# Performance work log

Hardware: AMD Instinct MI355X
Metric: run time of the kernel (lower is better)

Reference implementation:

```python
import jax, jax.numpy as jnp
import numpy as np
import math

B, T, D = 4, 4096, 1024
H, M = 16, 64
Dh = D // H


def _rope_tables(head_dim, max_seq_len, base=10000):
    inv_freq = 1.0 / (base ** (np.arange(0, head_dim, 2, dtype=np.float32) / head_dim))
    t = np.arange(max_seq_len, dtype=np.float32)
    freqs = np.einsum('i,j->ij', t, inv_freq)  # [T, Dh/2]
    cos = np.cos(freqs)
    sin = np.sin(freqs)
    # interleave (c, c) pairwise -> [T, Dh]
    cos = np.stack((cos, cos), axis=-1).reshape(max_seq_len, head_dim)
    sin = np.stack((sin, sin), axis=-1).reshape(max_seq_len, head_dim)
    return jnp.asarray(cos), jnp.asarray(sin)


def setup_inputs() -> dict:
    key = jax.random.key(0)
    ks = jax.random.split(key, 6)
    s = 1.0 / math.sqrt(D)
    x = jax.random.normal(ks[0], (B, T, D), dtype=jnp.float32)
    Wq = jnp.clip(jax.random.normal(ks[1], (D, D)) * s, -2 * s, 2 * s).astype(jnp.float32)
    Wk = jnp.clip(jax.random.normal(ks[2], (D, D)) * s, -2 * s, 2 * s).astype(jnp.float32)
    Wv = jnp.clip(jax.random.normal(ks[3], (D, D)) * s, -2 * s, 2 * s).astype(jnp.float32)
    Wo = jnp.clip(jax.random.normal(ks[4], (D, D)) * s, -2 * s, 2 * s).astype(jnp.float32)
    latent_code = (jax.random.normal(ks[5], (H, M, Dh)) * 0.02).astype(jnp.float32)
    rope_cos, rope_sin = _rope_tables(Dh, T)
    mask = jnp.ones((B, 1, T, 1), dtype=jnp.int32)
    return {'x': x, 'Wq': Wq, 'Wk': Wk, 'Wv': Wv, 'Wo': Wo,
            'latent_code': latent_code, 'rope_cos': rope_cos,
            'rope_sin': rope_sin, 'mask': mask}


def _rotate(x):
    # (x1, x2) pairs -> (-x2, x1), interleaved
    x2 = x.reshape(*x.shape[:-1], -1, 2)
    return jnp.stack((-x2[..., 1], x2[..., 0]), axis=-1).reshape(x.shape)


def reference(x, Wq, Wk, Wv, Wo, latent_code, rope_cos, rope_sin, mask):
    Bc, Tc, Dc = x.shape
    scale = 1.0 / math.sqrt(Dh)
    # projections -> [B, H, T, Dh]
    q = (x @ Wq.T).reshape(Bc, Tc, H, Dh).transpose(0, 2, 1, 3)
    k = (x @ Wk.T).reshape(Bc, Tc, H, Dh).transpose(0, 2, 1, 3)
    v = (x @ Wv.T).reshape(Bc, Tc, H, Dh).transpose(0, 2, 1, 3)
    cos = rope_cos[:Tc][None, None]  # [1,1,T,Dh]
    sin = rope_sin[:Tc][None, None]
    q = q * cos + _rotate(q) * sin
    k = k * cos + _rotate(k) * sin
    # Stage 1: token -> latent assignment, softmax over tokens (axis=2)
    assign_logits = jnp.einsum('bhtd,hmd->bhtm', k, latent_code) * scale
    assign_logits = jnp.where(mask == 0, -jnp.inf, assign_logits)
    assign = jax.nn.softmax(assign_logits, axis=2)
    k_lat = jnp.einsum('bhtm,bhtd->bhmd', assign, k)
    v_lat = jnp.einsum('bhtm,bhtd->bhmd', assign, v)
    # Stage 2: query attends to latents, softmax over latents (axis=-1)
    att2 = jnp.einsum('bhtd,bhmd->bhtm', q, k_lat) * scale
    p2 = jax.nn.softmax(att2, axis=-1)
    out = jnp.einsum('bhtm,bhmd->bhtd', p2, v_lat)
    out = out.transpose(0, 2, 1, 3).reshape(Bc, Tc, Dc)
    return out @ Wo.T
```

## Files before the change

kernel.cpp:

```cpp
#include <hip/hip_runtime.h>
#include <hip/hip_bf16.h>
#include <stdint.h>


#define DEV static __device__ __forceinline__

using short8 = __attribute__((ext_vector_type(8))) short;
using f32x4  = __attribute__((ext_vector_type(4))) float;

#define ZERO4 (f32x4){0.f, 0.f, 0.f, 0.f}

DEV float bf2f(unsigned short u) {
  union { unsigned int i; float f; } c; c.i = ((unsigned int)u) << 16; return c.f;
}
DEV unsigned short f2bf(float f) {
  __hip_bfloat16 h = __float2bfloat16(f);
  unsigned short u; __builtin_memcpy(&u, &h, 2); return u;
}
DEV f32x4 mfma16(short8 a, short8 b, f32x4 c) {
  return __builtin_amdgcn_mfma_f32_16x16x32_bf16(a, b, c, 0, 0, 0);
}
#define GLOAD_LDS16(G, L) __builtin_amdgcn_global_load_lds( \
    (const __attribute__((address_space(1))) void*)(G),     \
    (__attribute__((address_space(3))) void*)(L), 16, 0, 0)

__global__ void cvt_all(const float* __restrict__ x,
                        const float* __restrict__ Wq, const float* __restrict__ Wk,
                        const float* __restrict__ Wv, const float* __restrict__ Wo,
                        __hip_bfloat16* __restrict__ xb,
                        __hip_bfloat16* __restrict__ Wb) {
  const int bid = blockIdx.x;
  const float* src;
  __hip_bfloat16* dst;
  int base;
  if (bid < 16384) {
    src = x; dst = xb; base = bid;
  } else {
    const int k = (bid - 16384) >> 10;
    src = (k == 0) ? Wq : (k == 1) ? Wk : (k == 2) ? Wv : Wo;
    dst = Wb + (size_t)k * 1048576;
    base = (bid - 16384) & 1023;
  }
  const int i = (base * 256 + threadIdx.x) * 4;
  const float4 v = *(const float4*)(src + i);
  ushort4 o;
  o.x = f2bf(v.x); o.y = f2bf(v.y); o.z = f2bf(v.z); o.w = f2bf(v.w);
  *(ushort4*)(dst + i) = o;
}

#define GEMM_CORE(A_, B_, K_)                                                     \
  __shared__ __hip_bfloat16 As[2][256 * 64];                                      \
  __shared__ __hip_bfloat16 Bs[2][256 * 64];                                      \
  const int tid = threadIdx.x;                                                    \
  const int w = tid >> 6, l = tid & 63;                                           \
  const int lr = l & 15, lg = l >> 4;                                             \
  const int rowA0 = blockIdx.x * 256;                                             \
  const int colB0 = blockIdx.y * 256;                                             \
  const int srow = w * 8 + (l >> 3);                                              \
  const int skk  = (((l & 7) ^ (l >> 3)) * 8);                                    \
  const __hip_bfloat16* Ab = A_ + (size_t)(rowA0 + srow) * K_ + skk;              \
  const __hip_bfloat16* Bb = B_ + (size_t)(colB0 + srow) * K_ + skk;              \
  f32x4 acc[8][4];                                                                \
  _Pragma("unroll")                                                               \
  for (int i = 0; i < 8; ++i)                                                     \
    _Pragma("unroll")                                                             \
    for (int j = 0; j < 4; ++j) acc[i][j] = ZERO4;                                \
  const int wr = (w >> 2) * 128;                                                  \
  const int wc = (w & 3) * 64;                                                    \
  const int NT = K_ >> 6;                                                         \
  {                                                                               \
    const int k0s = 0;                                                            \
    _Pragma("unroll")                                                             \
    for (int i = 0; i < 4; ++i) {                                                 \
      GLOAD_LDS16(Ab + (size_t)(i * 64) * K_ + k0s, &As[0][i * 4096 + w * 512]);  \
      GLOAD_LDS16(Bb + (size_t)(i * 64) * K_ + k0s, &Bs[0][i * 4096 + w * 512]);  \
    }                                                                             \
  }                                                                               \
  for (int kt = 0; kt < NT; ++kt) {                                               \
    const int cur = kt & 1;                                                       \
    if (kt + 1 < NT) {                                                            \
      const int k0s = (kt + 1) * 64;                                              \
      _Pragma("unroll")                                                           \
      for (int i = 0; i < 4; ++i) {                                               \
        GLOAD_LDS16(Ab + (size_t)(i * 64) * K_ + k0s, &As[cur ^ 1][i * 4096 + w * 512]); \
        GLOAD_LDS16(Bb + (size_t)(i * 64) * K_ + k0s, &Bs[cur ^ 1][i * 4096 + w * 512]); \
      }                                                                           \
      asm volatile("s_waitcnt vmcnt(8)" ::: "memory");                            \
    } else {                                                                      \
      asm volatile("s_waitcnt vmcnt(0)" ::: "memory");                            \
    }                                                                             \
    __builtin_amdgcn_s_barrier();                                                 \
    __builtin_amdgcn_s_setprio(1);                                                \
    _Pragma("unroll")                                                             \
    for (int s = 0; s < 2; ++s) {                                                 \
      short8 fa[8], fb[4];                                                        \
      _Pragma("unroll")                                                           \
      for (int i = 0; i < 8; ++i)                                                 \
        fa[i] = *(const short8*)&As[cur][(wr + i * 16 + lr) * 64 +                \
                                         (((s * 4 + lg) ^ (lr & 7)) * 8)];        \
      _Pragma("unroll")                                                           \
      for (int j = 0; j < 4; ++j)                                                 \
        fb[j] = *(const short8*)&Bs[cur][(wc + j * 16 + lr) * 64 +                \
                                         (((s * 4 + lg) ^ (lr & 7)) * 8)];        \
      _Pragma("unroll")                                                           \
      for (int i = 0; i < 8; ++i)                                                 \
        _Pragma("unroll")                                                         \
        for (int j = 0; j < 4; ++j)                                               \
          acc[i][j] = mfma16(fa[i], fb[j], acc[i][j]);                            \
    }                                                                             \
    __builtin_amdgcn_s_setprio(0);                                                \
    __builtin_amdgcn_s_barrier();                                                 \
  }

__global__ __launch_bounds__(512, 2)
void gemm_qkv(const __hip_bfloat16* __restrict__ A,
              const __hip_bfloat16* __restrict__ Bt,
              __hip_bfloat16* __restrict__ qb,
              __hip_bfloat16* __restrict__ kb,
              __hip_bfloat16* __restrict__ kT,
              __hip_bfloat16* __restrict__ vT,
              const float* __restrict__ cosT, const float* __restrict__ sinT) {
  GEMM_CORE(A, Bt, 1024)
  const int r0 = rowA0 + wr + lg * 4;
  const int c0 = colB0 + wc + lr;
  const int panel = blockIdx.y >> 2;
  if (panel < 2) {
#pragma unroll
    for (int i = 0; i < 8; ++i)
#pragma unroll
      for (int j = 0; j < 4; ++j)
#pragma unroll
        for (int r = 0; r < 4; ++r) {
          const int m = r0 + i * 16 + r;
          const int n = c0 + j * 16;
          const int t = m & 4095, d = n & 63;
          const float c = cosT[t * 64 + d];
          const float s = sinT[t * 64 + d];
          const float v = acc[i][j][r];
          const float other = __shfl_xor(v, 1, 64);
          acc[i][j][r] = v * c + ((n & 1) ? other : -other) * s;
        }
  }
  if (panel < 2) {
    __hip_bfloat16* Cn = (panel == 0) ? qb : kb;
#pragma unroll
    for (int i = 0; i < 8; ++i)
#pragma unroll
      for (int j = 0; j < 4; ++j)
#pragma unroll
        for (int r = 0; r < 4; ++r) {
          const int nn = (c0 + j * 16) & 1023;
          Cn[(size_t)(r0 + i * 16 + r) * 1024 + nn] = __float2bfloat16(acc[i][j][r]);
        }
  }
  if (panel >= 1) {
    __hip_bfloat16* Ct = (panel == 1) ? kT : vT;
#pragma unroll
    for (int i = 0; i < 8; ++i)
#pragma unroll
      for (int j = 0; j < 4; ++j) {
        const int m0 = r0 + i * 16;
        const int nn = (c0 + j * 16) & 1023;
        const size_t row = (size_t)(((m0 >> 12) * 16 + (nn >> 6)) * 64 + (nn & 63));
        ushort4 pk;
        pk.x = f2bf(acc[i][j][0]); pk.y = f2bf(acc[i][j][1]);
        pk.z = f2bf(acc[i][j][2]); pk.w = f2bf(acc[i][j][3]);
        *(ushort4*)&Ct[row * 4096 + (m0 & 4095)] = pk;
      }
  }
}

__global__ __launch_bounds__(512, 2)
void gemm_out(const __hip_bfloat16* __restrict__ A,
              const __hip_bfloat16* __restrict__ Bt,
              float* __restrict__ Cout) {
  GEMM_CORE(A, Bt, 1024)
  const int r0 = rowA0 + wr + lg * 4;
  const int c0 = colB0 + wc + lr;
#pragma unroll
  for (int i = 0; i < 8; ++i)
#pragma unroll
    for (int j = 0; j < 4; ++j)
#pragma unroll
      for (int r = 0; r < 4; ++r)
        Cout[(size_t)(r0 + i * 16 + r) * 1024 + (c0 + j * 16)] = acc[i][j][r];
}

__global__ __launch_bounds__(256)
void stage1_expS(const __hip_bfloat16* __restrict__ kmat,
                 const float* __restrict__ latent,
                 const int* __restrict__ mask,
                 __hip_bfloat16* __restrict__ P,
                 float* __restrict__ psum) {
  const int bh = blockIdx.x, chunk = blockIdx.y;
  const int b = bh >> 4, h = bh & 15;
  const int tid = threadIdx.x, w = tid >> 6, l = tid & 63;
  const int lr = l & 15, lg = l >> 4;
  short8 la[4][2];
#pragma unroll
  for (int n = 0; n < 4; ++n)
#pragma unroll
    for (int s = 0; s < 2; ++s) {
      const float* lp = &latent[((size_t)h * 64 + n * 16 + lr) * 64 + s * 32 + lg * 8];
      short8 f;
#pragma unroll
      for (int j = 0; j < 8; ++j) f[j] = (short)f2bf(lp[j]);
      la[n][s] = f;
    }
  float sm[16];
#pragma unroll
  for (int i = 0; i < 16; ++i) sm[i] = 0.f;
  for (int tile = 0; tile < 8; ++tile) {
    const int t = chunk * 512 + tile * 64 + w * 16 + lr;
    const __hip_bfloat16* kp = &kmat[((size_t)(b * 4096 + t) * 16 + h) * 64 + lg * 8];
    const short8 kb0 = *(const short8*)kp;
    const short8 kb1 = *(const short8*)(kp + 32);
    const bool live = (mask[b * 4096 + t] != 0);
    f32x4 acc[4];
#pragma unroll
    for (int n = 0; n < 4; ++n) {
      acc[n] = ZERO4;
      acc[n] = mfma16(la[n][0], kb0, acc[n]);
      acc[n] = mfma16(la[n][1], kb1, acc[n]);
    }
#pragma unroll
    for (int n = 0; n < 4; ++n)
#pragma unroll
      for (int r = 0; r < 4; ++r) {
        const float e = live ? __expf(acc[n][r] * 0.125f) : 0.f;
        const int m = n * 16 + lg * 4 + r;
        ((unsigned short*)P)[((size_t)bh * 64 + m) * 4096 + t] = f2bf(e);
        sm[n * 4 + r] += e;
      }
  }
#pragma unroll
  for (int o = 1; o < 16; o <<= 1)
#pragma unroll
    for (int i = 0; i < 16; ++i) sm[i] += __shfl_xor(sm[i], o, 64);
  if (lr == 0) {
    const size_t pb = ((size_t)(bh * 8 + chunk) * 4 + w) * 64;
#pragma unroll
    for (int n = 0; n < 4; ++n)
#pragma unroll
      for (int r = 0; r < 4; ++r)
        psum[pb + n * 16 + lg * 4 + r] = sm[n * 4 + r];
  }
}

__global__ void denom_inv(const float* __restrict__ psum, float* __restrict__ cinv) {
  const int i = blockIdx.x * 256 + threadIdx.x;
  if (i >= 4096) return;
  const int bh = i >> 6, m = i & 63;
  float sm = 0.f;
#pragma unroll
  for (int c = 0; c < 32; ++c)
    sm += psum[((size_t)bh * 32 + c) * 64 + m];
  cinv[i] = 1.f / sm;
}

__global__ __launch_bounds__(256)
void latgemm7(const __hip_bfloat16* __restrict__ P,
              const __hip_bfloat16* __restrict__ kT,
              const __hip_bfloat16* __restrict__ vT,
              float* __restrict__ partials) {
  const int bh = blockIdx.x;
  const int tid = threadIdx.x, w = tid >> 6, l = tid & 63;
  const int slice = blockIdx.y * 4 + w;
  const int lr = l & 15;
  const int lk = (l >> 4) * 8;
  const size_t base = (size_t)bh * 64 * 4096;
  f32x4 ak[4][4], av[4][4];
#pragma unroll
  for (int i = 0; i < 4; ++i)
#pragma unroll
    for (int j = 0; j < 4; ++j) { ak[i][j] = ZERO4; av[i][j] = ZERO4; }
  for (int ks = 0; ks < 8; ++ks) {
    const int t = slice * 256 + ks * 32 + lk;
    short8 fp[4], fk[4], fv[4];
#pragma unroll
    for (int i = 0; i < 4; ++i) {
      const size_t ro = base + (size_t)(i * 16 + lr) * 4096 + t;
      fp[i] = *(const short8*)&P[ro];
      fk[i] = *(const short8*)&kT[ro];
      fv[i] = *(const short8*)&vT[ro];
    }
#pragma unroll
    for (int i = 0; i < 4; ++i)
#pragma unroll
      for (int j = 0; j < 4; ++j) {
        ak[i][j] = mfma16(fp[i], fk[j], ak[i][j]);
        av[i][j] = mfma16(fv[i], fp[j], av[i][j]);
      }
  }
  float* pk = partials + ((size_t)(slice * 64 + bh)) * 8192;
#pragma unroll
  for (int i = 0; i < 4; ++i)
#pragma unroll
    for (int j = 0; j < 4; ++j)
#pragma unroll
      for (int r = 0; r < 4; ++r) {
        const int row = i * 16 + 4 * (l >> 4) + r;
        const int col = j * 16 + lr;
        pk[(size_t)row * 64 + col]        = ak[i][j][r];
        pk[4096 + (size_t)row * 64 + col] = av[i][j][r];
      }
}

__global__ void latreduce2(const float* __restrict__ partials,
                           const float* __restrict__ cinv,
                           __hip_bfloat16* __restrict__ k_lat,
                           __hip_bfloat16* __restrict__ v_latT) {
  const int i = blockIdx.x * 256 + threadIdx.x;
  const int bh = i >> 13, off = i & 8191;
  float sm = 0.f;
#pragma unroll
  for (int c = 0; c < 16; ++c)
    sm += partials[((size_t)(c * 64 + bh)) * 8192 + off];
  const int m = (off < 4096) ? (off >> 6) : (off & 63);
  sm *= cinv[bh * 64 + m];
  if (off < 4096) k_lat[(size_t)bh * 4096 + off] = __float2bfloat16(sm);
  else            v_latT[(size_t)bh * 4096 + (off - 4096)] = __float2bfloat16(sm);
}

__global__ __launch_bounds__(256)
void stage2_attn(const __hip_bfloat16* __restrict__ q,
                 const __hip_bfloat16* __restrict__ k_lat,
                 const __hip_bfloat16* __restrict__ v_latT,
                 __hip_bfloat16* __restrict__ attn) {
  __shared__ unsigned short Pl[4][16][64];
  const int bid = blockIdx.x;
  const int bh = bid >> 6, tt = (bid & 63) * 64;
  const int b = bh >> 4, h = bh & 15;
  const int tid = threadIdx.x, w = tid >> 6, l = tid & 63;
  const size_t qoff = ((size_t)(b * 4096 + tt + w * 16 + (l & 15)) * 16 + h) * 64;
  const short8 a0 = *(const short8*)&q[qoff + (l >> 4) * 8];
  const short8 a1 = *(const short8*)&q[qoff + 32 + (l >> 4) * 8];
  f32x4 att[4];
#pragma unroll
  for (int n = 0; n < 4; ++n) att[n] = ZERO4;
#pragma unroll
  for (int n = 0; n < 4; ++n) {
    const __hip_bfloat16* kl = &k_lat[((size_t)bh * 64 + n * 16 + (l & 15)) * 64];
    const short8 b0 = *(const short8*)&kl[(l >> 4) * 8];
    const short8 b1 = *(const short8*)&kl[32 + (l >> 4) * 8];
    att[n] = mfma16(a0, b0, att[n]);
    att[n] = mfma16(a1, b1, att[n]);
  }
  float p[4][4];
#pragma unroll
  for (int r = 0; r < 4; ++r) {
    const float v0 = att[0][r] * 0.125f, v1 = att[1][r] * 0.125f;
    const float v2 = att[2][r] * 0.125f, v3 = att[3][r] * 0.125f;
    float mxv = fmaxf(fmaxf(v0, v1), fmaxf(v2, v3));
#pragma unroll
    for (int o = 1; o < 16; o <<= 1) mxv = fmaxf(mxv, __shfl_xor(mxv, o, 64));
    const float e0 = __expf(v0 - mxv), e1 = __expf(v1 - mxv);
    const float e2 = __expf(v2 - mxv), e3 = __expf(v3 - mxv);
    float sum = e0 + e1 + e2 + e3;
#pragma unroll
    for (int o = 1; o < 16; o <<= 1) sum += __shfl_xor(sum, o, 64);
    const float inv = 1.f / sum;
    p[0][r] = e0 * inv; p[1][r] = e1 * inv; p[2][r] = e2 * inv; p[3][r] = e3 * inv;
  }
#pragma unroll
  for (int n = 0; n < 4; ++n)
#pragma unroll
    for (int r = 0; r < 4; ++r) {
      const int row = 4 * (l >> 4) + r;
      const int col = n * 16 + (l & 15);
      Pl[w][row][col ^ ((row & 7) << 3)] = f2bf(p[n][r]);
    }
  __syncthreads();
  const int arow = l & 15;
  const short8 pa0 = *(const short8*)&Pl[w][arow][(((l >> 4) + 0) ^ (arow & 7)) * 8];
  const short8 pa1 = *(const short8*)&Pl[w][arow][(((l >> 4) + 4) ^ (arow & 7)) * 8];
  f32x4 ov[4];
#pragma unroll
  for (int n = 0; n < 4; ++n) ov[n] = ZERO4;
#pragma unroll
  for (int n = 0; n < 4; ++n) {
    const __hip_bfloat16* vt = &v_latT[((size_t)bh * 64 + n * 16 + (l & 15)) * 64];
    const short8 b0 = *(const short8*)&vt[(l >> 4) * 8];
    const short8 b1 = *(const short8*)&vt[32 + (l >> 4) * 8];
    ov[n] = mfma16(pa0, b0, ov[n]);
    ov[n] = mfma16(pa1, b1, ov[n]);
  }
#pragma unroll
  for (int n = 0; n < 4; ++n) {
    const int d = n * 16 + (l & 15);
#pragma unroll
    for (int r = 0; r < 4; ++r) {
      const int trow = tt + w * 16 + 4 * (l >> 4) + r;
      attn[((size_t)(b * 4096 + trow) * 16 + h) * 64 + d] = __float2bfloat16(ov[n][r]);
    }
  }
}

extern "C" void kernel_launch(void* const* d_in, const int* in_sizes, int n_in,
                              void* d_out, int out_size, void* d_ws, size_t ws_size,
                              hipStream_t stream) {
  const float* x      = (const float*)d_in[0];
  const float* Wq     = (const float*)d_in[1];
  const float* Wk     = (const float*)d_in[2];
  const float* Wv     = (const float*)d_in[3];
  const float* Wo     = (const float*)d_in[4];
  const float* latent = (const float*)d_in[5];
  const float* cosT   = (const float*)d_in[6];
  const float* sinT   = (const float*)d_in[7];
  const int*   mask   = (const int*)d_in[8];

  char* ws = (char*)d_ws;
  __hip_bfloat16* xb = (__hip_bfloat16*)ws;
  __hip_bfloat16* Wb = (__hip_bfloat16*)(ws + 33554432);
  __hip_bfloat16* qb = (__hip_bfloat16*)(ws + 41943040);
  __hip_bfloat16* kb = (__hip_bfloat16*)(ws + 75497472);
  __hip_bfloat16* kT = (__hip_bfloat16*)(ws + 109051904);
  __hip_bfloat16* vT = (__hip_bfloat16*)(ws + 142606336);
  char* tail = ws + 176160768;
  float* psum = (float*)tail;
  float* cinv = psum + 131072;
  __hip_bfloat16* k_lat  = (__hip_bfloat16*)(cinv + 4096);
  __hip_bfloat16* v_latT = k_lat + 262144;
  float* partials = (float*)kb;
  __hip_bfloat16* P    = xb;
  __hip_bfloat16* attn = qb;

  cvt_all<<<20480, 256, 0, stream>>>(x, Wq, Wk, Wv, Wo, xb, Wb);

  dim3 gq(64, 12);
  gemm_qkv<<<gq, 512, 0, stream>>>(xb, Wb, qb, kb, kT, vT, cosT, sinT);

  dim3 sg(64, 8);
  stage1_expS<<<sg, 256, 0, stream>>>(kb, latent, mask, P, psum);
  denom_inv<<<16, 256, 0, stream>>>(psum, cinv);

  dim3 lg(64, 4);
  latgemm7<<<lg, 256, 0, stream>>>(P, kT, vT, partials);
  latreduce2<<<2048, 256, 0, stream>>>(partials, cinv, k_lat, v_latT);

  stage2_attn<<<4096, 256, 0, stream>>>(qb, k_lat, v_latT, attn);

  dim3 go(64, 4);
  gemm_out<<<go, 512, 0, stream>>>(attn, Wb + 3 * 1048576, (float*)d_out);
}
```

Measured before the change: 294.5 us.

## Shrink GEMM tiles to 128x128 with 4 waves and fold denom_inv into latreduce

The shared GEMM core now uses 128x128 output tiles computed by 256-thread blocks, where it used 256x256 tiles on 512 threads. The grids for the QKV and output projections are enlarged to match, and the panel index is adjusted. Separately, the denom_inv kernel is removed: each latreduce2 block computes the 64 inverse softmax denominators into shared memory itself, which saves one launch. Smaller tiles give more blocks and better CU fill on the 256-CU device, at the cost of lower arithmetic intensity per block and more redundant global loads. The denominators are now recomputed redundantly in every latreduce block.

```diff
diff --git a/kernel.cpp b/kernel.cpp
--- a/kernel.cpp
+++ b/kernel.cpp
@@ -49,31 +49,30 @@
 }
 
 #define GEMM_CORE(A_, B_, K_)                                                     \
-  __shared__ __hip_bfloat16 As[2][256 * 64];                                      \
-  __shared__ __hip_bfloat16 Bs[2][256 * 64];                                      \
+  __shared__ __hip_bfloat16 As[2][128 * 64];                                      \
+  __shared__ __hip_bfloat16 Bs[2][128 * 64];                                      \
   const int tid = threadIdx.x;                                                    \
   const int w = tid >> 6, l = tid & 63;                                           \
   const int lr = l & 15, lg = l >> 4;                                             \
-  const int rowA0 = blockIdx.x * 256;                                             \
-  const int colB0 = blockIdx.y * 256;                                             \
+  const int rowA0 = blockIdx.x * 128;                                             \
+  const int colB0 = blockIdx.y * 128;                                             \
   const int srow = w * 8 + (l >> 3);                                              \
   const int skk  = (((l & 7) ^ (l >> 3)) * 8);                                    \
   const __hip_bfloat16* Ab = A_ + (size_t)(rowA0 + srow) * K_ + skk;              \
   const __hip_bfloat16* Bb = B_ + (size_t)(colB0 + srow) * K_ + skk;              \
-  f32x4 acc[8][4];                                                                \
+  f32x4 acc[4][4];                                                                \
   _Pragma("unroll")                                                               \
-  for (int i = 0; i < 8; ++i)                                                     \
+  for (int i = 0; i < 4; ++i)                                                     \
     _Pragma("unroll")                                                             \
     for (int j = 0; j < 4; ++j) acc[i][j] = ZERO4;                                \
-  const int wr = (w >> 2) * 128;                                                  \
-  const int wc = (w & 3) * 64;                                                    \
+  const int wr = (w >> 1) * 64;                                                   \
+  const int wc = (w & 1) * 64;                                                    \
   const int NT = K_ >> 6;                                                         \
   {                                                                               \
-    const int k0s = 0;                                                            \
     _Pragma("unroll")                                                             \
     for (int i = 0; i < 4; ++i) {                                                 \
-      GLOAD_LDS16(Ab + (size_t)(i * 64) * K_ + k0s, &As[0][i * 4096 + w * 512]);  \
-      GLOAD_LDS16(Bb + (size_t)(i * 64) * K_ + k0s, &Bs[0][i * 4096 + w * 512]);  \
+      GLOAD_LDS16(Ab + (size_t)(i * 32) * K_, &As[0][i * 2048 + w * 512]);        \
+      GLOAD_LDS16(Bb + (size_t)(i * 32) * K_, &Bs[0][i * 2048 + w * 512]);        \
     }                                                                             \
   }                                                                               \
   for (int kt = 0; kt < NT; ++kt) {                                               \
@@ -82,8 +81,8 @@
       const int k0s = (kt + 1) * 64;                                              \
       _Pragma("unroll")                                                           \
       for (int i = 0; i < 4; ++i) {                                               \
-        GLOAD_LDS16(Ab + (size_t)(i * 64) * K_ + k0s, &As[cur ^ 1][i * 4096 + w * 512]); \
-        GLOAD_LDS16(Bb + (size_t)(i * 64) * K_ + k0s, &Bs[cur ^ 1][i * 4096 + w * 512]); \
+        GLOAD_LDS16(Ab + (size_t)(i * 32) * K_ + k0s, &As[cur ^ 1][i * 2048 + w * 512]); \
+        GLOAD_LDS16(Bb + (size_t)(i * 32) * K_ + k0s, &Bs[cur ^ 1][i * 2048 + w * 512]); \
       }                                                                           \
       asm volatile("s_waitcnt vmcnt(8)" ::: "memory");                            \
     } else {                                                                      \
@@ -93,9 +92,9 @@
     __builtin_amdgcn_s_setprio(1);                                                \
     _Pragma("unroll")                                                             \
     for (int s = 0; s < 2; ++s) {                                                 \
-      short8 fa[8], fb[4];                                                        \
+      short8 fa[4], fb[4];                                                        \
       _Pragma("unroll")                                                           \
-      for (int i = 0; i < 8; ++i)                                                 \
+      for (int i = 0; i < 4; ++i)                                                 \
         fa[i] = *(const short8*)&As[cur][(wr + i * 16 + lr) * 64 +                \
                                          (((s * 4 + lg) ^ (lr & 7)) * 8)];        \
       _Pragma("unroll")                                                           \
@@ -103,7 +102,7 @@
         fb[j] = *(const short8*)&Bs[cur][(wc + j * 16 + lr) * 64 +                \
                                          (((s * 4 + lg) ^ (lr & 7)) * 8)];        \
       _Pragma("unroll")                                                           \
-      for (int i = 0; i < 8; ++i)                                                 \
+      for (int i = 0; i < 4; ++i)                                                 \
         _Pragma("unroll")                                                         \
         for (int j = 0; j < 4; ++j)                                               \
           acc[i][j] = mfma16(fa[i], fb[j], acc[i][j]);                            \
@@ -112,7 +111,7 @@
     __builtin_amdgcn_s_barrier();                                                 \
   }
 
-__global__ __launch_bounds__(512, 2)
+__global__ __launch_bounds__(256)
 void gemm_qkv(const __hip_bfloat16* __restrict__ A,
               const __hip_bfloat16* __restrict__ Bt,
               __hip_bfloat16* __restrict__ qb,
@@ -123,10 +122,10 @@
   GEMM_CORE(A, Bt, 1024)
   const int r0 = rowA0 + wr + lg * 4;
   const int c0 = colB0 + wc + lr;
-  const int panel = blockIdx.y >> 2;
+  const int panel = blockIdx.y >> 3;
   if (panel < 2) {
 #pragma unroll
-    for (int i = 0; i < 8; ++i)
+    for (int i = 0; i < 4; ++i)
 #pragma unroll
       for (int j = 0; j < 4; ++j)
 #pragma unroll
@@ -144,7 +143,7 @@
   if (panel < 2) {
     __hip_bfloat16* Cn = (panel == 0) ? qb : kb;
 #pragma unroll
-    for (int i = 0; i < 8; ++i)
+    for (int i = 0; i < 4; ++i)
 #pragma unroll
       for (int j = 0; j < 4; ++j)
 #pragma unroll
@@ -156,7 +155,7 @@
   if (panel >= 1) {
     __hip_bfloat16* Ct = (panel == 1) ? kT : vT;
 #pragma unroll
-    for (int i = 0; i < 8; ++i)
+    for (int i = 0; i < 4; ++i)
 #pragma unroll
       for (int j = 0; j < 4; ++j) {
         const int m0 = r0 + i * 16;
@@ -170,7 +169,7 @@
   }
 }
 
-__global__ __launch_bounds__(512, 2)
+__global__ __launch_bounds__(256)
 void gemm_out(const __hip_bfloat16* __restrict__ A,
               const __hip_bfloat16* __restrict__ Bt,
               float* __restrict__ Cout) {
@@ -178,7 +177,7 @@
   const int r0 = rowA0 + wr + lg * 4;
   const int c0 = colB0 + wc + lr;
 #pragma unroll
-  for (int i = 0; i < 8; ++i)
+  for (int i = 0; i < 4; ++i)
 #pragma unroll
     for (int j = 0; j < 4; ++j)
 #pragma unroll
@@ -245,17 +244,6 @@
       for (int r = 0; r < 4; ++r)
         psum[pb + n * 16 + lg * 4 + r] = sm[n * 4 + r];
   }
-}
-
-__global__ void denom_inv(const float* __restrict__ psum, float* __restrict__ cinv) {
-  const int i = blockIdx.x * 256 + threadIdx.x;
-  if (i >= 4096) return;
-  const int bh = i >> 6, m = i & 63;
-  float sm = 0.f;
-#pragma unroll
-  for (int c = 0; c < 32; ++c)
-    sm += psum[((size_t)bh * 32 + c) * 64 + m];
-  cinv[i] = 1.f / sm;
 }
 
 __global__ __launch_bounds__(256)
@@ -307,17 +295,29 @@
 }
 
 __global__ void latreduce2(const float* __restrict__ partials,
-                           const float* __restrict__ cinv,
+                           const float* __restrict__ psum,
                            __hip_bfloat16* __restrict__ k_lat,
                            __hip_bfloat16* __restrict__ v_latT) {
-  const int i = blockIdx.x * 256 + threadIdx.x;
-  const int bh = i >> 13, off = i & 8191;
+  __shared__ float sci[64];
+  const int bid = blockIdx.x;
+  const int bh = bid >> 5;
+  const int tid = threadIdx.x;
+  if (tid < 64) {
+    float s = 0.f;
+#pragma unroll
+    for (int c = 0; c < 32; ++c)
+      s += psum[((size_t)bh * 32 + c) * 64 + tid];
+    sci[tid] = 1.f / s;
+  }
+  __syncthreads();
+  const int i = bid * 256 + tid;
+  const int off = i & 8191;
   float sm = 0.f;
 #pragma unroll
   for (int c = 0; c < 16; ++c)
     sm += partials[((size_t)(c * 64 + bh)) * 8192 + off];
   const int m = (off < 4096) ? (off >> 6) : (off & 63);
-  sm *= cinv[bh * 64 + m];
+  sm *= sci[m];
   if (off < 4096) k_lat[(size_t)bh * 4096 + off] = __float2bfloat16(sm);
   else            v_latT[(size_t)bh * 4096 + (off - 4096)] = __float2bfloat16(sm);
 }
@@ -418,8 +418,7 @@
   __hip_bfloat16* vT = (__hip_bfloat16*)(ws + 142606336);
   char* tail = ws + 176160768;
   float* psum = (float*)tail;
-  float* cinv = psum + 131072;
-  __hip_bfloat16* k_lat  = (__hip_bfloat16*)(cinv + 4096);
+  __hip_bfloat16* k_lat  = (__hip_bfloat16*)(psum + 131072);
   __hip_bfloat16* v_latT = k_lat + 262144;
   float* partials = (float*)kb;
   __hip_bfloat16* P    = xb;
@@ -427,19 +426,18 @@
 
   cvt_all<<<20480, 256, 0, stream>>>(x, Wq, Wk, Wv, Wo, xb, Wb);
 
-  dim3 gq(64, 12);
-  gemm_qkv<<<gq, 512, 0, stream>>>(xb, Wb, qb, kb, kT, vT, cosT, sinT);
+  dim3 gq(128, 24);
+  gemm_qkv<<<gq, 256, 0, stream>>>(xb, Wb, qb, kb, kT, vT, cosT, sinT);
 
   dim3 sg(64, 8);
   stage1_expS<<<sg, 256, 0, stream>>>(kb, latent, mask, P, psum);
-  denom_inv<<<16, 256, 0, stream>>>(psum, cinv);
 
   dim3 lg(64, 4);
   latgemm7<<<lg, 256, 0, stream>>>(P, kT, vT, partials);
-  latreduce2<<<2048, 256, 0, stream>>>(partials, cinv, k_lat, v_latT);
+  latreduce2<<<2048, 256, 0, stream>>>(partials, psum, k_lat, v_latT);
 
   stage2_attn<<<4096, 256, 0, stream>>>(qb, k_lat, v_latT, attn);
 
-  dim3 go(64, 4);
-  gemm_out<<<go, 512, 0, stream>>>(attn, Wb + 3 * 1048576, (float*)d_out);
-}
+  dim3 go(128, 8);
+  gemm_out<<<go, 256, 0, stream>>>(attn, Wb + 3 * 1048576, (float*)d_out);
+}
```

Result: slower. 316.6 us (+7.5%).

## Fuse stage-1 latent assignment into QKV GEMM epilogue and fold denominator into reduce

Applied to the files above, without the earlier changes.

The K-panel epilogue of the QKV GEMM now stages the RoPE'd K tile in shared memory and computes the latent logits, exp and partial softmax sums there. This removes the separate stage1 kernel and the row-major K buffer write and re-read. The denominator kernel is also removed: latreduce2 now sums psum per block into shared memory. The cost is a longer, register-heavier epilogue on the K panels, which creates load imbalance across the GEMM grid. Each reduce block also redundantly re-sums psum.

```diff
diff --git a/kernel.cpp b/kernel.cpp
--- a/kernel.cpp
+++ b/kernel.cpp
@@ -116,9 +116,12 @@
 void gemm_qkv(const __hip_bfloat16* __restrict__ A,
               const __hip_bfloat16* __restrict__ Bt,
               __hip_bfloat16* __restrict__ qb,
-              __hip_bfloat16* __restrict__ kb,
               __hip_bfloat16* __restrict__ kT,
               __hip_bfloat16* __restrict__ vT,
+              const float* __restrict__ latent,
+              const int* __restrict__ mask,
+              __hip_bfloat16* __restrict__ P,
+              float* __restrict__ psum,
               const float* __restrict__ cosT, const float* __restrict__ sinT) {
   GEMM_CORE(A, Bt, 1024)
   const int r0 = rowA0 + wr + lg * 4;
@@ -141,8 +144,7 @@
           acc[i][j][r] = v * c + ((n & 1) ? other : -other) * s;
         }
   }
-  if (panel < 2) {
-    __hip_bfloat16* Cn = (panel == 0) ? qb : kb;
+  if (panel == 0) {
 #pragma unroll
     for (int i = 0; i < 8; ++i)
 #pragma unroll
@@ -150,7 +152,7 @@
 #pragma unroll
         for (int r = 0; r < 4; ++r) {
           const int nn = (c0 + j * 16) & 1023;
-          Cn[(size_t)(r0 + i * 16 + r) * 1024 + nn] = __float2bfloat16(acc[i][j][r]);
+          qb[(size_t)(r0 + i * 16 + r) * 1024 + nn] = __float2bfloat16(acc[i][j][r]);
         }
   }
   if (panel >= 1) {
@@ -168,6 +170,76 @@
         *(ushort4*)&Ct[row * 4096 + (m0 & 4095)] = pk;
       }
   }
+  if (panel == 1) {
+    const int hh = w & 3;
+    __hip_bfloat16* Hb = (hh < 2) ? As[hh] : Bs[hh - 2];
+#pragma unroll
+    for (int i = 0; i < 8; ++i)
+#pragma unroll
+      for (int j = 0; j < 4; ++j)
+#pragma unroll
+        for (int r = 0; r < 4; ++r) {
+          const int tl = wr + lg * 4 + i * 16 + r;
+          const int d  = lr + j * 16;
+          Hb[tl * 64 + ((((d >> 3) ^ (tl & 7)) << 3) | (d & 7))] =
+              __float2bfloat16(acc[i][j][r]);
+        }
+    __syncthreads();
+    const int hg = ((colB0 & 1023) >> 6) + hh;
+    const int b  = rowA0 >> 12;
+    const int t0 = rowA0 & 4095;
+    const int bh = b * 16 + hg;
+    short8 la[4][2];
+#pragma unroll
+    for (int n = 0; n < 4; ++n)
+#pragma unroll
+      for (int s = 0; s < 2; ++s) {
+        const float* lp = &latent[((size_t)hg * 64 + n * 16 + lr) * 64 + s * 32 + lg * 8];
+        short8 f;
+#pragma unroll
+        for (int j = 0; j < 8; ++j) f[j] = (short)f2bf(lp[j]);
+        la[n][s] = f;
+      }
+    float sm2[16];
+#pragma unroll
+    for (int i = 0; i < 16; ++i) sm2[i] = 0.f;
+    const int thalf = (w >> 2) * 128;
+    for (int tt2 = 0; tt2 < 8; ++tt2) {
+      const int tl = thalf + tt2 * 16 + lr;
+      const short8 kf0 = *(const short8*)&Hb[tl * 64 + (((0 + lg) ^ (tl & 7)) << 3)];
+      const short8 kf1 = *(const short8*)&Hb[tl * 64 + (((4 + lg) ^ (tl & 7)) << 3)];
+      const bool live = (mask[b * 4096 + t0 + tl] != 0);
+      f32x4 a2[4];
+#pragma unroll
+      for (int n = 0; n < 4; ++n) {
+        a2[n] = ZERO4;
+        a2[n] = mfma16(la[n][0], kf0, a2[n]);
+        a2[n] = mfma16(la[n][1], kf1, a2[n]);
+      }
+#pragma unroll
+      for (int n = 0; n < 4; ++n)
+#pragma unroll
+        for (int r = 0; r < 4; ++r) {
+          const float e = live ? __expf(a2[n][r] * 0.125f) : 0.f;
+          const int m = n * 16 + lg * 4 + r;
+          ((unsigned short*)P)[((size_t)bh * 64 + m) * 4096 + t0 + tl] = f2bf(e);
+          sm2[n * 4 + r] += e;
+        }
+    }
+#pragma unroll
+    for (int o = 1; o < 16; o <<= 1)
+#pragma unroll
+      for (int i = 0; i < 16; ++i) sm2[i] += __shfl_xor(sm2[i], o, 64);
+    if (lr == 0) {
+      const int pchunk = (t0 >> 8) * 2 + (w >> 2);
+      const size_t pb = ((size_t)bh * 32 + pchunk) * 64;
+#pragma unroll
+      for (int n = 0; n < 4; ++n)
+#pragma unroll
+        for (int r = 0; r < 4; ++r)
+          psum[pb + n * 16 + lg * 4 + r] = sm2[n * 4 + r];
+    }
+  }
 }
 
 __global__ __launch_bounds__(512, 2)
@@ -184,78 +256,6 @@
 #pragma unroll
       for (int r = 0; r < 4; ++r)
         Cout[(size_t)(r0 + i * 16 + r) * 1024 + (c0 + j * 16)] = acc[i][j][r];
-}
-
-__global__ __launch_bounds__(256)
-void stage1_expS(const __hip_bfloat16* __restrict__ kmat,
-                 const float* __restrict__ latent,
-                 const int* __restrict__ mask,
-                 __hip_bfloat16* __restrict__ P,
-                 float* __restrict__ psum) {
-  const int bh = blockIdx.x, chunk = blockIdx.y;
-  const int b = bh >> 4, h = bh & 15;
-  const int tid = threadIdx.x, w = tid >> 6, l = tid & 63;
-  const int lr = l & 15, lg = l >> 4;
-  short8 la[4][2];
-#pragma unroll
-  for (int n = 0; n < 4; ++n)
-#pragma unroll
-    for (int s = 0; s < 2; ++s) {
-      const float* lp = &latent[((size_t)h * 64 + n * 16 + lr) * 64 + s * 32 + lg * 8];
-      short8 f;
-#pragma unroll
-      for (int j = 0; j < 8; ++j) f[j] = (short)f2bf(lp[j]);
-      la[n][s] = f;
-    }
-  float sm[16];
-#pragma unroll
-  for (int i = 0; i < 16; ++i) sm[i] = 0.f;
-  for (int tile = 0; tile < 8; ++tile) {
-    const int t = chunk * 512 + tile * 64 + w * 16 + lr;
-    const __hip_bfloat16* kp = &kmat[((size_t)(b * 4096 + t) * 16 + h) * 64 + lg * 8];
-    const short8 kb0 = *(const short8*)kp;
-    const short8 kb1 = *(const short8*)(kp + 32);
-    const bool live = (mask[b * 4096 + t] != 0);
-    f32x4 acc[4];
-#pragma unroll
-    for (int n = 0; n < 4; ++n) {
-      acc[n] = ZERO4;
-      acc[n] = mfma16(la[n][0], kb0, acc[n]);
-      acc[n] = mfma16(la[n][1], kb1, acc[n]);
-    }
-#pragma unroll
-    for (int n = 0; n < 4; ++n)
-#pragma unroll
-      for (int r = 0; r < 4; ++r) {
-        const float e = live ? __expf(acc[n][r] * 0.125f) : 0.f;
-        const int m = n * 16 + lg * 4 + r;
-        ((unsigned short*)P)[((size_t)bh * 64 + m) * 4096 + t] = f2bf(e);
-        sm[n * 4 + r] += e;
-      }
-  }
-#pragma unroll
-  for (int o = 1; o < 16; o <<= 1)
-#pragma unroll
-    for (int i = 0; i < 16; ++i) sm[i] += __shfl_xor(sm[i], o, 64);
-  if (lr == 0) {
-    const size_t pb = ((size_t)(bh * 8 + chunk) * 4 + w) * 64;
-#pragma unroll
-    for (int n = 0; n < 4; ++n)
-#pragma unroll
-      for (int r = 0; r < 4; ++r)
-        psum[pb + n * 16 + lg * 4 + r] = sm[n * 4 + r];
-  }
-}
-
-__global__ void denom_inv(const float* __restrict__ psum, float* __restrict__ cinv) {
-  const int i = blockIdx.x * 256 + threadIdx.x;
-  if (i >= 4096) return;
-  const int bh = i >> 6, m = i & 63;
-  float sm = 0.f;
-#pragma unroll
-  for (int c = 0; c < 32; ++c)
-    sm += psum[((size_t)bh * 32 + c) * 64 + m];
-  cinv[i] = 1.f / sm;
 }
 
 __global__ __launch_bounds__(256)
@@ -307,17 +307,29 @@
 }
 
 __global__ void latreduce2(const float* __restrict__ partials,
-                           const float* __restrict__ cinv,
+                           const float* __restrict__ psum,
                            __hip_bfloat16* __restrict__ k_lat,
                            __hip_bfloat16* __restrict__ v_latT) {
-  const int i = blockIdx.x * 256 + threadIdx.x;
-  const int bh = i >> 13, off = i & 8191;
+  __shared__ float sci[64];
+  const int bid = blockIdx.x;
+  const int bh = bid >> 5;
+  const int tid = threadIdx.x;
+  if (tid < 64) {
+    float s = 0.f;
+#pragma unroll
+    for (int c = 0; c < 32; ++c)
+      s += psum[((size_t)bh * 32 + c) * 64 + tid];
+    sci[tid] = 1.f / s;
+  }
+  __syncthreads();
+  const int i = bid * 256 + tid;
+  const int off = i & 8191;
   float sm = 0.f;
 #pragma unroll
   for (int c = 0; c < 16; ++c)
     sm += partials[((size_t)(c * 64 + bh)) * 8192 + off];
   const int m = (off < 4096) ? (off >> 6) : (off & 63);
-  sm *= cinv[bh * 64 + m];
+  sm *= sci[m];
   if (off < 4096) k_lat[(size_t)bh * 4096 + off] = __float2bfloat16(sm);
   else            v_latT[(size_t)bh * 4096 + (off - 4096)] = __float2bfloat16(sm);
 }
@@ -418,25 +430,20 @@
   __hip_bfloat16* vT = (__hip_bfloat16*)(ws + 142606336);
   char* tail = ws + 176160768;
   float* psum = (float*)tail;
-  float* cinv = psum + 131072;
-  __hip_bfloat16* k_lat  = (__hip_bfloat16*)(cinv + 4096);
+  __hip_bfloat16* k_lat  = (__hip_bfloat16*)(psum + 131072);
   __hip_bfloat16* v_latT = k_lat + 262144;
-  float* partials = (float*)kb;
-  __hip_bfloat16* P    = xb;
+  __hip_bfloat16* P = kb;
+  float* partials = (float*)xb;
   __hip_bfloat16* attn = qb;
 
   cvt_all<<<20480, 256, 0, stream>>>(x, Wq, Wk, Wv, Wo, xb, Wb);
 
   dim3 gq(64, 12);
-  gemm_qkv<<<gq, 512, 0, stream>>>(xb, Wb, qb, kb, kT, vT, cosT, sinT);
-
-  dim3 sg(64, 8);
-  stage1_expS<<<sg, 256, 0, stream>>>(kb, latent, mask, P, psum);
-  denom_inv<<<16, 256, 0, stream>>>(psum, cinv);
+  gemm_qkv<<<gq, 512, 0, stream>>>(xb, Wb, qb, kT, vT, latent, mask, P, psum, cosT, sinT);
 
   dim3 lg(64, 4);
   latgemm7<<<lg, 256, 0, stream>>>(P, kT, vT, partials);
-  latreduce2<<<2048, 256, 0, stream>>>(partials, cinv, k_lat, v_latT);
+  latreduce2<<<2048, 256, 0, stream>>>(partials, psum, k_lat, v_latT);
 
   stage2_attn<<<4096, 256, 0, stream>>>(qb, k_lat, v_latT, attn);
 
```

After: 293.2 us. About the same (-0.4%).
